# Performance work log

Hardware: AMD Instinct MI355X
Metric: run time of the kernel (lower is better)

The kernel has to match this reference:

```python
import jax, jax.numpy as jnp
import numpy as np

EPS = 1e-08


def _center(K):
    # H K H with H = I - 11^T/n, expressed as O(n^2) double mean-subtraction
    rm = K.mean(axis=-1, keepdims=True)
    cm = K.mean(axis=-2, keepdims=True)
    tm = K.mean(axis=(-1, -2), keepdims=True)
    return K - rm - cm + tm


def setup_inputs() -> dict:
    key = jax.random.key(0)
    k1, k2 = jax.random.split(key)
    L, B, n, d = 5, 8, 1024, 64
    teacher = jax.random.normal(k1, (L, B, n, d), dtype=jnp.float32)
    student = jax.random.normal(k2, (L, B, n, d), dtype=jnp.float32)
    return {"teacher": teacher, "student": student}


def reference(teacher, student):
    # teacher, student: [L, B, n, d]  (internal=True, dim>=3 branch)
    cX = _center(jnp.einsum('lbnd,lbmd->lbnm', teacher, teacher))  # [L,B,n,n]
    cY = _center(jnp.einsum('lbnd,lbmd->lbnm', student, student))  # [L,B,n,n]
    hsic_xy = jnp.sum(cX * cY, axis=(-1, -2))  # [L,B]
    var_x = jnp.sqrt(jnp.sum(cX * cX, axis=(-1, -2)))  # [L,B]
    var_y = jnp.sqrt(jnp.sum(cY * cY, axis=(-1, -2)))  # [L,B]
    ratio = jnp.abs(hsic_xy / (var_x * var_y))  # [L,B]
    loss_per_layer = -jnp.log(ratio.mean(axis=-1) + EPS)  # [L]
    return loss_per_layer.mean()  # sum over layers / length
```

## Files before the change

### kernel.cpp

```cpp
#include <hip/hip_runtime.h>
#include <math.h>

#define LL 5
#define BB 8
#define NN 1024
#define DD 64
#define LB (LL * BB)
#define ZC (2 * DD)
#define CHUNK 128
#define NCH (NN / CHUNK)

typedef short short8 __attribute__((ext_vector_type(8)));
typedef float floatx4 __attribute__((ext_vector_type(4)));

__device__ __forceinline__ unsigned short f2bf(float f) {
    union { float f; unsigned u; } v; v.f = f;
    const unsigned u = v.u;
    return (unsigned short)((u + 0x7FFFu + ((u >> 16) & 1u)) >> 16);
}
__device__ __forceinline__ float bf2f(unsigned short h) {
    union { unsigned u; float f; } v; v.u = ((unsigned)h) << 16; return v.f;
}

__device__ __forceinline__ short8 read_frag(const short* Zt, int t, int lane, int k0) {
    const int c = t + (lane & 15);
    const int o = (k0 >> 3) + (lane >> 4);
    return *(const short8*)(Zt + c * 128 + ((o ^ (c & 15)) << 3));
}

__global__ __launch_bounds__(512) void gram_fused(const float* __restrict__ X,
                                                  const float* __restrict__ Y,
                                                  float* __restrict__ R) {
    __shared__ short Zt[2][CHUNK * ZC];
    __shared__ float csum_sh[4][ZC];
    __shared__ float stot[ZC];
    __shared__ float red[4];

    const int lb = blockIdx.x;
    const int tid = threadIdx.x;
    const int c = tid & 127;
    const int qq = tid >> 7;

    const float* src = (c < DD) ? (X + (size_t)lb * NN * DD + c)
                                : (Y + (size_t)lb * NN * DD + (c - DD));

    const int lane = tid & 63, w = tid >> 6;
    const int qd = w & 3, hf = w >> 2;
    const int wr = (qd >> 1) << 6;
    const int wc_ = (qd & 1) << 6;

    floatx4 acc[4][4];
#pragma unroll
    for (int i = 0; i < 4; ++i)
#pragma unroll
        for (int j = 0; j < 4; ++j)
            acc[i][j] = (floatx4){0.f, 0.f, 0.f, 0.f};
    float csum = 0.0f;

    {
        short* Bn = Zt[0];
#pragma unroll
        for (int j = 0; j < 16; ++j) {
            const int kp = qq * 16 + j;
            const float v0 = src[(size_t)(2 * kp) * DD];
            const float v1 = src[(size_t)(2 * kp + 1) * DD];
            const unsigned short b0 = f2bf(v0), b1 = f2bf(v1);
            csum += bf2f(b0) + bf2f(b1);
            const unsigned val = (unsigned)b0 | ((unsigned)b1 << 16);
            const int o = kp >> 2, dw = kp & 3;
            *(unsigned*)((char*)Bn + (c << 8) + (((o ^ (c & 15)) << 4) + (dw << 2))) = val;
        }
    }
    __syncthreads();

    for (int ch = 0; ch < NCH; ++ch) {
        const short* B = Zt[ch & 1];
        if (ch + 1 < NCH) {
            const int rbase = (ch + 1) * CHUNK;
            short* Bn = Zt[(ch + 1) & 1];
#pragma unroll
            for (int j = 0; j < 16; ++j) {
                const int kp = qq * 16 + j;
                const float v0 = src[(size_t)(rbase + 2 * kp) * DD];
                const float v1 = src[(size_t)(rbase + 2 * kp + 1) * DD];
                const unsigned short b0 = f2bf(v0), b1 = f2bf(v1);
                csum += bf2f(b0) + bf2f(b1);
                const unsigned val = (unsigned)b0 | ((unsigned)b1 << 16);
                const int o = kp >> 2, dw = kp & 3;
                *(unsigned*)((char*)Bn + (c << 8) + (((o ^ (c & 15)) << 4) + (dw << 2))) = val;
            }
        }
#pragma unroll
        for (int s = 0; s < 2; ++s) {
            const int k0 = hf * 64 + s * 32;
            short8 af[4], bfr[4];
#pragma unroll
            for (int i = 0; i < 4; ++i) af[i] = read_frag(B, wr + i * 16, lane, k0);
#pragma unroll
            for (int j = 0; j < 4; ++j) bfr[j] = read_frag(B, wc_ + j * 16, lane, k0);
#pragma unroll
            for (int i = 0; i < 4; ++i)
#pragma unroll
                for (int j = 0; j < 4; ++j)
                    acc[i][j] = __builtin_amdgcn_mfma_f32_16x16x32_bf16(af[i], bfr[j], acc[i][j], 0, 0, 0);
        }
        __syncthreads();
    }

    csum_sh[qq][c] = csum;
    float* scr = (float*)Zt;
    __syncthreads();

    const int g = lane >> 4, cl = lane & 15;
    if (hf == 0) {
#pragma unroll
        for (int i = 0; i < 4; ++i)
#pragma unroll
            for (int j = 0; j < 4; ++j)
#pragma unroll
                for (int r = 0; r < 4; ++r)
                    scr[qd * 4096 + (i * 16 + g * 4 + r) * 64 + (j * 16 + cl)] = acc[i][j][r];
    }
    if (tid < ZC)
        stot[tid] = csum_sh[0][tid] + csum_sh[1][tid] + csum_sh[2][tid] + csum_sh[3][tid];
    __syncthreads();

    if (hf == 1 && qd != 2) {
        const float inv_n = 1.0f / (float)NN;
        float sq = 0.0f;
#pragma unroll
        for (int i = 0; i < 4; ++i)
#pragma unroll
            for (int j = 0; j < 4; ++j) {
                const int col = wc_ + j * 16 + cl;
                const float sc = stot[col] * inv_n;
#pragma unroll
                for (int r = 0; r < 4; ++r) {
                    const int row = wr + i * 16 + g * 4 + r;
                    const float v = acc[i][j][r] + scr[qd * 4096 + (i * 16 + g * 4 + r) * 64 + (j * 16 + cl)];
                    const float cv = v - stot[row] * sc;
                    sq += cv * cv;
                }
            }
#pragma unroll
        for (int off = 32; off; off >>= 1) sq += __shfl_down(sq, off);
        if (lane == 0) red[qd] = sq;
    }
    __syncthreads();
    if (tid == 0) {
        const float vxx = red[0], hxy = red[1], vyy = red[3];
        R[lb] = fabsf(hxy / (sqrtf(vxx) * sqrtf(vyy)));
    }
}

__global__ void final_kernel(const float* __restrict__ R, float* __restrict__ out) {
    const int tid = threadIdx.x;
    float v = (tid < LB) ? R[tid] : 0.0f;
    v += __shfl_xor(v, 1);
    v += __shfl_xor(v, 2);
    v += __shfl_xor(v, 4);
    float loss = 0.0f;
#pragma unroll
    for (int l = 0; l < LL; ++l) {
        const float sl = __shfl(v, l * BB);
        loss += -logf(sl * (1.0f / (float)BB) + 1e-8f);
    }
    if (tid == 0) out[0] = loss * (1.0f / (float)LL);
}

extern "C" void kernel_launch(void* const* d_in, const int* in_sizes, int n_in,
                              void* d_out, int out_size, void* d_ws, size_t ws_size,
                              hipStream_t stream) {
    const float* teacher = (const float*)d_in[0];
    const float* student = (const float*)d_in[1];
    float* R = (float*)d_ws;

    gram_fused<<<LB, 512, 0, stream>>>(teacher, student, R);
    final_kernel<<<1, 64, 0, stream>>>(R, (float*)d_out);
}
```

Measured before the change: 81.57 us.

## Split 128x128 Gram into 32x32 tiles across blocks with atomic accumulation

Each (l,b) pair is now handled by ten blocks, one per unique upper-triangle 32x32 tile of the combined 128x128 feature Gram, instead of a single 512-thread block. This raises the grid from 40 to 400 blocks to fill more compute units. Symmetric off-diagonal tiles are weighted by 2, and the partial squared sums are combined with atomicAdd into a zeroed workspace. In exchange, each block re-reads and re-converts input columns that other blocks also load, and the launch gains a memset plus float atomics whose summation order is nondeterministic.

```diff
diff --git a/kernel.cpp b/kernel.cpp
--- a/kernel.cpp
+++ b/kernel.cpp
@@ -6,9 +6,9 @@
 #define NN 1024
 #define DD 64
 #define LB (LL * BB)
-#define ZC (2 * DD)
-#define CHUNK 128
-#define NCH (NN / CHUNK)
+#define KC 128
+#define NCH (NN / KC)
+#define NTILE 10
 
 typedef short short8 __attribute__((ext_vector_type(8)));
 typedef float floatx4 __attribute__((ext_vector_type(4)));
@@ -22,140 +22,138 @@
     union { unsigned u; float f; } v; v.u = ((unsigned)h) << 16; return v.f;
 }
 
-__device__ __forceinline__ short8 read_frag(const short* Zt, int t, int lane, int k0) {
-    const int c = t + (lane & 15);
-    const int o = (k0 >> 3) + (lane >> 4);
-    return *(const short8*)(Zt + c * 128 + ((o ^ (c & 15)) << 3));
-}
+__global__ __launch_bounds__(256) void gram_tiled(const float* __restrict__ X,
+                                                  const float* __restrict__ Y,
+                                                  float* __restrict__ Acc) {
+    static const int   GIa[NTILE]  = {0, 0, 1, 2, 2, 3, 0, 0, 1, 1};
+    static const int   GJa[NTILE]  = {0, 1, 1, 2, 3, 3, 2, 3, 2, 3};
+    static const int   CATa[NTILE] = {0, 0, 0, 2, 2, 2, 1, 1, 1, 1};
+    static const float WTa[NTILE]  = {1.f, 2.f, 1.f, 1.f, 2.f, 1.f, 1.f, 1.f, 1.f, 1.f};
 
-__global__ __launch_bounds__(512) void gram_fused(const float* __restrict__ X,
-                                                  const float* __restrict__ Y,
-                                                  float* __restrict__ R) {
-    __shared__ short Zt[2][CHUNK * ZC];
-    __shared__ float csum_sh[4][ZC];
-    __shared__ float stot[ZC];
-    __shared__ float red[4];
+    __shared__ short Zt[2][64 * KC];
+    __shared__ float csum_scr[16][64];
+    __shared__ float stot[64];
+    __shared__ float redw[4];
 
-    const int lb = blockIdx.x;
+    const int bid = blockIdx.x;
+    const int lb = bid % LB;
+    const int t  = bid / LB;
+    const int gi = GIa[t], gj = GJa[t], cat = CATa[t];
+    const float wt = WTa[t];
+
     const int tid = threadIdx.x;
-    const int c = tid & 127;
-    const int qq = tid >> 7;
+    const int lane = tid & 63, wv = tid >> 6;
 
-    const float* src = (c < DD) ? (X + (size_t)lb * NN * DD + c)
-                                : (Y + (size_t)lb * NN * DD + (c - DD));
+    const int c4 = tid & 15;
+    const int cc = c4 & 7;
+    const int isJ = c4 >> 3;
+    const int grp = isJ ? gj : gi;
+    const int Lc = isJ * 32 + cc * 4;
+    const float4* gp4 = (const float4*)(((grp < 2) ? X : Y) + (size_t)lb * NN * DD);
+    const int colb = (grp & 1) * 8 + cc;
 
-    const int lane = tid & 63, w = tid >> 6;
-    const int qd = w & 3, hf = w >> 2;
-    const int wr = (qd >> 1) << 6;
-    const int wc_ = (qd & 1) << 6;
+    float csump[4] = {0.f, 0.f, 0.f, 0.f};
 
-    floatx4 acc[4][4];
+    auto stage = [&](int ch, short* buf) {
 #pragma unroll
-    for (int i = 0; i < 4; ++i)
+        for (int s = 0; s < 4; ++s) {
+            const int kp = (tid >> 4) + s * 16;
+            const size_t row = (size_t)ch * KC + 2 * kp;
+            const float4 f0 = gp4[row * 16 + colb];
+            const float4 f1 = gp4[(row + 1) * 16 + colb];
+            const float a0[4] = {f0.x, f0.y, f0.z, f0.w};
+            const float a1[4] = {f1.x, f1.y, f1.z, f1.w};
 #pragma unroll
-        for (int j = 0; j < 4; ++j)
-            acc[i][j] = (floatx4){0.f, 0.f, 0.f, 0.f};
-    float csum = 0.0f;
+            for (int e = 0; e < 4; ++e) {
+                const unsigned short b0 = f2bf(a0[e]), b1 = f2bf(a1[e]);
+                csump[e] += bf2f(b0) + bf2f(b1);
+                const int c = Lc + e;
+                const int dw = c * 64 + ((((kp >> 2)) ^ (c & 15)) << 2) + (kp & 3);
+                ((unsigned*)buf)[dw] = (unsigned)b0 | ((unsigned)b1 << 16);
+            }
+        }
+    };
 
+    floatx4 acc[2][2];
+#pragma unroll
+    for (int i = 0; i < 2; ++i)
+#pragma unroll
+        for (int j = 0; j < 2; ++j) acc[i][j] = (floatx4){0.f, 0.f, 0.f, 0.f};
+
+    auto compute = [&](const short* buf) {
+        const int o = wv * 4 + (lane >> 4);
+        short8 af[2], bfr[2];
+#pragma unroll
+        for (int i = 0; i < 2; ++i) {
+            const int ca = i * 16 + (lane & 15);
+            af[i] = *(const short8*)(buf + ca * 128 + ((o ^ (ca & 15)) << 3));
+            const int cb = 32 + i * 16 + (lane & 15);
+            bfr[i] = *(const short8*)(buf + cb * 128 + ((o ^ (cb & 15)) << 3));
+        }
+#pragma unroll
+        for (int i = 0; i < 2; ++i)
+#pragma unroll
+            for (int j = 0; j < 2; ++j)
+                acc[i][j] = __builtin_amdgcn_mfma_f32_16x16x32_bf16(af[i], bfr[j], acc[i][j], 0, 0, 0);
+    };
+
+    stage(0, Zt[0]);
+    __syncthreads();
+    for (int ch = 0; ch < NCH; ++ch) {
+        if (ch + 1 < NCH) stage(ch + 1, Zt[(ch + 1) & 1]);
+        compute(Zt[ch & 1]);
+        __syncthreads();
+    }
+
+    float* scr = (float*)Zt;
     {
-        short* Bn = Zt[0];
+        const int g = lane >> 4, cl = lane & 15;
 #pragma unroll
-        for (int j = 0; j < 16; ++j) {
-            const int kp = qq * 16 + j;
-            const float v0 = src[(size_t)(2 * kp) * DD];
-            const float v1 = src[(size_t)(2 * kp + 1) * DD];
-            const unsigned short b0 = f2bf(v0), b1 = f2bf(v1);
-            csum += bf2f(b0) + bf2f(b1);
-            const unsigned val = (unsigned)b0 | ((unsigned)b1 << 16);
-            const int o = kp >> 2, dw = kp & 3;
-            *(unsigned*)((char*)Bn + (c << 8) + (((o ^ (c & 15)) << 4) + (dw << 2))) = val;
-        }
+        for (int i = 0; i < 2; ++i)
+#pragma unroll
+            for (int j = 0; j < 2; ++j)
+#pragma unroll
+                for (int r = 0; r < 4; ++r)
+                    scr[wv * 1024 + (i * 16 + g * 4 + r) * 32 + (j * 16 + cl)] = acc[i][j][r];
+    }
+#pragma unroll
+    for (int e = 0; e < 4; ++e) csum_scr[tid >> 4][Lc + e] = csump[e];
+    __syncthreads();
+    if (tid < 64) {
+        float s = 0.f;
+#pragma unroll
+        for (int i = 0; i < 16; ++i) s += csum_scr[i][tid];
+        stot[tid] = s;
     }
     __syncthreads();
 
-    for (int ch = 0; ch < NCH; ++ch) {
-        const short* B = Zt[ch & 1];
-        if (ch + 1 < NCH) {
-            const int rbase = (ch + 1) * CHUNK;
-            short* Bn = Zt[(ch + 1) & 1];
+    float sq = 0.f;
+    const float inv_n = 1.0f / (float)NN;
 #pragma unroll
-            for (int j = 0; j < 16; ++j) {
-                const int kp = qq * 16 + j;
-                const float v0 = src[(size_t)(rbase + 2 * kp) * DD];
-                const float v1 = src[(size_t)(rbase + 2 * kp + 1) * DD];
-                const unsigned short b0 = f2bf(v0), b1 = f2bf(v1);
-                csum += bf2f(b0) + bf2f(b1);
-                const unsigned val = (unsigned)b0 | ((unsigned)b1 << 16);
-                const int o = kp >> 2, dw = kp & 3;
-                *(unsigned*)((char*)Bn + (c << 8) + (((o ^ (c & 15)) << 4) + (dw << 2))) = val;
-            }
-        }
+    for (int e = 0; e < 4; ++e) {
+        const int idx = tid * 4 + e;
+        const int m = idx >> 5, nn2 = idx & 31;
+        const float g = scr[idx] + scr[1024 + idx] + scr[2048 + idx] + scr[3072 + idx];
+        const float cv = g - stot[m] * stot[32 + nn2] * inv_n;
+        sq += cv * cv;
+    }
 #pragma unroll
-        for (int s = 0; s < 2; ++s) {
-            const int k0 = hf * 64 + s * 32;
-            short8 af[4], bfr[4];
-#pragma unroll
-            for (int i = 0; i < 4; ++i) af[i] = read_frag(B, wr + i * 16, lane, k0);
-#pragma unroll
-            for (int j = 0; j < 4; ++j) bfr[j] = read_frag(B, wc_ + j * 16, lane, k0);
-#pragma unroll
-            for (int i = 0; i < 4; ++i)
-#pragma unroll
-                for (int j = 0; j < 4; ++j)
-                    acc[i][j] = __builtin_amdgcn_mfma_f32_16x16x32_bf16(af[i], bfr[j], acc[i][j], 0, 0, 0);
-        }
-        __syncthreads();
-    }
-
-    csum_sh[qq][c] = csum;
-    float* scr = (float*)Zt;
+    for (int off = 32; off; off >>= 1) sq += __shfl_down(sq, off);
+    if (lane == 0) redw[wv] = sq;
     __syncthreads();
-
-    const int g = lane >> 4, cl = lane & 15;
-    if (hf == 0) {
-#pragma unroll
-        for (int i = 0; i < 4; ++i)
-#pragma unroll
-            for (int j = 0; j < 4; ++j)
-#pragma unroll
-                for (int r = 0; r < 4; ++r)
-                    scr[qd * 4096 + (i * 16 + g * 4 + r) * 64 + (j * 16 + cl)] = acc[i][j][r];
-    }
-    if (tid < ZC)
-        stot[tid] = csum_sh[0][tid] + csum_sh[1][tid] + csum_sh[2][tid] + csum_sh[3][tid];
-    __syncthreads();
-
-    if (hf == 1 && qd != 2) {
-        const float inv_n = 1.0f / (float)NN;
-        float sq = 0.0f;
-#pragma unroll
-        for (int i = 0; i < 4; ++i)
-#pragma unroll
-            for (int j = 0; j < 4; ++j) {
-                const int col = wc_ + j * 16 + cl;
-                const float sc = stot[col] * inv_n;
-#pragma unroll
-                for (int r = 0; r < 4; ++r) {
-                    const int row = wr + i * 16 + g * 4 + r;
-                    const float v = acc[i][j][r] + scr[qd * 4096 + (i * 16 + g * 4 + r) * 64 + (j * 16 + cl)];
-                    const float cv = v - stot[row] * sc;
-                    sq += cv * cv;
-                }
-            }
-#pragma unroll
-        for (int off = 32; off; off >>= 1) sq += __shfl_down(sq, off);
-        if (lane == 0) red[qd] = sq;
-    }
-    __syncthreads();
-    if (tid == 0) {
-        const float vxx = red[0], hxy = red[1], vyy = red[3];
-        R[lb] = fabsf(hxy / (sqrtf(vxx) * sqrtf(vyy)));
-    }
+    if (tid == 0)
+        atomicAdd(&Acc[lb * 4 + cat], wt * (redw[0] + redw[1] + redw[2] + redw[3]));
 }
 
-__global__ void final_kernel(const float* __restrict__ R, float* __restrict__ out) {
+__global__ void final_kernel(const float* __restrict__ Acc, float* __restrict__ out) {
     const int tid = threadIdx.x;
-    float v = (tid < LB) ? R[tid] : 0.0f;
+    float v = 0.0f;
+    if (tid < LB) {
+        const float a = Acc[tid * 4 + 0];
+        const float h = Acc[tid * 4 + 1];
+        const float b = Acc[tid * 4 + 2];
+        v = fabsf(h / (sqrtf(a) * sqrtf(b)));
+    }
     v += __shfl_xor(v, 1);
     v += __shfl_xor(v, 2);
     v += __shfl_xor(v, 4);
@@ -173,8 +171,9 @@
                               hipStream_t stream) {
     const float* teacher = (const float*)d_in[0];
     const float* student = (const float*)d_in[1];
-    float* R = (float*)d_ws;
+    float* Acc = (float*)d_ws;
 
-    gram_fused<<<LB, 512, 0, stream>>>(teacher, student, R);
-    final_kernel<<<1, 64, 0, stream>>>(R, (float*)d_out);
+    hipMemsetAsync(Acc, 0, LB * 4 * sizeof(float), stream);
+    gram_tiled<<<LB * NTILE, 256, 0, stream>>>(teacher, student, Acc);
+    final_kernel<<<1, 64, 0, stream>>>(Acc, (float*)d_out);
 }
```

New measurement: 83.31 us. 1.02x slower.
